# Kernel tuning notes

Hardware: AMD Instinct MI355X
Metric: run time of the kernel (lower is better)

Reference implementation:

```python
import jax, jax.numpy as jnp
import numpy as np

N_DIM, D_SKETCH, M_COLS = 8192, 1024, 4096


def setup_inputs() -> dict:
    key = jax.random.key(0)
    kM, kD, kP = jax.random.split(key, 3)
    M = jax.random.normal(kM, (N_DIM, M_COLS), dtype=jnp.float32)
    # Rademacher signs, exactly as 2*(rand > 0.5).float() - 1
    D = 2.0 * (jax.random.uniform(kD, (N_DIM,)) > 0.5).astype(jnp.float32) - 1.0
    # np.random.choice(N, d) samples with replacement -> plain randint
    P = jax.random.randint(kP, (D_SKETCH,), 0, N_DIM)
    return {"M": M, "D": D, "P": P}


def _idct_rows(X, rows):
    # torch_dct.idct with norm=None along the last axis, evaluated only at the
    # output positions `rows` (identical values to full idct followed by gather):
    #   x[n] = (1/N) * ( X[...,0]/2 + sum_{k=1}^{N-1} X[...,k] * cos(pi*(2n+1)*k/(2N)) )
    N = X.shape[-1]
    k = jnp.arange(N, dtype=jnp.float32)
    w = jnp.where(k == 0, 0.5, 1.0) / N                      # DCT-III weights / N
    n = rows.astype(jnp.float32)
    ang = (jnp.pi / (2.0 * N)) * (2.0 * n[:, None] + 1.0) * k[None, :]
    C = jnp.cos(ang) * w[None, :]                            # [d, N]
    return jnp.einsum('dk,mk->md', C, X)                     # [m, d]


def reference(M, D, P):
    # SRFT sketch, 2-D branch, transpose=False:
    #   result = idct((D[:, None] * M).T).T[P, :]   ->  shape [d, m]
    X = D[:, None] * M                                       # sign flip, [N, m]
    out = _idct_rows(X.T, P)                                 # [m, d]
    return out.T                                             # [d, m]
```

## Files before the change

### kernel.cpp

```cpp
#include <hip/hip_runtime.h>

#define K_DIM 8192
#define M_OUT 1024
#define N_OUT 4096
#define BUFSZ 49152

typedef __attribute__((ext_vector_type(4))) float f32x4;
typedef __attribute__((ext_vector_type(8))) __bf16 bf16x8;
typedef __attribute__((ext_vector_type(2))) __bf16 bf16x2;
typedef __attribute__((ext_vector_type(8))) unsigned short u16x8;

__device__ __forceinline__ unsigned short f2bf(float x) {
  unsigned u = __builtin_bit_cast(unsigned, x);
  u += 0x7fffu + ((u >> 16) & 1u);
  return (unsigned short)(u >> 16);
}

__device__ __forceinline__ unsigned pack2(float a, float b) {
  bf16x2 v;
  v[0] = (__bf16)a;
  v[1] = (__bf16)b;
  return __builtin_bit_cast(unsigned, v);
}

__global__ __launch_bounds__(256) void build_c_kernel(
    const int* __restrict__ Pp, const float* __restrict__ Dp,
    unsigned short* __restrict__ Cm) {
  const int p = blockIdx.x;
  const int n2 = 2 * Pp[p] + 1;
  const int t = threadIdx.x;
#pragma unroll
  for (int ch = 0; ch < 4; ++ch) {
    const int kb = (ch << 11) + (t << 3);
    u16x8 o;
#pragma unroll
    for (int i = 0; i < 8; ++i) {
      const int k = kb + i;
      const unsigned tt = ((unsigned)(n2 * k)) & 32767u;
      const float cv = cosf((float)tt * 1.9174759848570515e-4f);
      const float wk = (k == 0) ? (0.5f / 8192.0f) : (1.0f / 8192.0f);
      o[i] = f2bf(cv * wk * Dp[k]);
    }
    *(u16x8*)(Cm + ((size_t)p << 13) + kb) = o;
  }
}

__global__ __launch_bounds__(512, 2) void gemm_kernel(
    const unsigned short* __restrict__ Cm, const float* __restrict__ Mp,
    float* __restrict__ outp, int kchunk, int nwg) {
  __shared__ __align__(16) char lds[2 * BUFSZ];

  const int id = blockIdx.x;
  const int chunk = nwg >> 3;
  const int sid = (id & 7) * chunk + (id >> 3);
  const int bz = sid & 1, bm = (sid >> 1) & 3, bn = sid >> 3;

  const int t = threadIdx.x;
  const int w = t >> 6, l = t & 63;
  const int wr = w >> 1, wc = w & 1;
  const int lg = l >> 4, lr = l & 15;
  const int k_begin = bz * kchunk;
  const int NT = kchunk >> 6;

  const int arow = t >> 3;
  const int acol = ((t & 7) << 4) ^ ((arow & 7) << 4);
  const char* Agl = (const char*)Cm + ((size_t)(bm * 256 + arow) << 14) +
                    ((size_t)k_begin << 1) + acol;
  auto stageA = [&](int nbuf, int tile) {
    char* d = (char*)lds + nbuf * BUFSZ + t * 16;
    const char* s = Agl + ((size_t)tile << 7);
#pragma unroll
    for (int i = 0; i < 4; ++i)
      __builtin_amdgcn_global_load_lds(
          (const __attribute__((address_space(1))) void*)(s + ((size_t)i << 20)),
          (__attribute__((address_space(3))) void*)(d + i * 8192), 16, 0, 0);
  };

  const int bk0 = w * 8 + (l >> 5) * 4;
  const int bn0 = (l & 31) * 4;
  const float* Bg = Mp + (size_t)k_begin * N_OUT + bn * 128 + bn0;
  auto loadB = [&](f32x4 (&r)[4], int tile) {
#pragma unroll
    for (int i = 0; i < 4; ++i)
      r[i] = *(const f32x4*)(Bg + (size_t)(tile * 64 + bk0 + i) * N_OUT);
  };
  auto writeB = [&](const f32x4 (&r)[4], int nbuf) {
#pragma unroll
    for (int nn = 0; nn < 4; ++nn) {
      const int n = bn0 + nn;
      const int sN = (n & 7) ^ ((n >> 2) & 7);
      uint2 pk;
      pk.x = pack2(r[0][nn], r[1][nn]);
      pk.y = pack2(r[2][nn], r[3][nn]);
      *(uint2*)(lds + nbuf * BUFSZ + 32768 + n * 128 + ((w ^ sN) << 4) +
                ((l >> 5) << 3)) = pk;
    }
  };

  const int sw = (lr & 7) << 4;
  const int xk0 = (lg << 4) ^ sw;
  const int xk1 = (64 + (lg << 4)) ^ sw;
  unsigned boff[2][4];
#pragma unroll
  for (int kk = 0; kk < 2; ++kk)
#pragma unroll
    for (int nf = 0; nf < 4; ++nf) {
      const int row = wc * 64 + nf * 16 + lr;
      const int sN = (row & 7) ^ ((row >> 2) & 7);
      boff[kk][nf] = 32768 + row * 128 + ((((kk << 2) | lg) ^ sN) << 4);
    }

  f32x4 acc[4][4] = {};
  bf16x8 Af[4];
  bf16x8 Bf[4];

  auto readA = [&](int nbuf, int xk) {
    const char* aBuf = (const char*)lds + nbuf * BUFSZ + wr * 8192 + lr * 128;
#pragma unroll
    for (int m = 0; m < 4; ++m)
      Af[m] = *(const bf16x8*)(aBuf + m * 2048 + xk);
  };
  auto readB = [&](int nbuf, int kk) {
#pragma unroll
    for (int nf = 0; nf < 4; ++nf)
      Bf[nf] = *(const bf16x8*)(lds + nbuf * BUFSZ + boff[kk][nf]);
  };
  auto mm = [&]() {
    __builtin_amdgcn_s_setprio(1);
#pragma unroll
    for (int m = 0; m < 4; ++m)
#pragma unroll
      for (int nf = 0; nf < 4; ++nf)
        acc[m][nf] = __builtin_amdgcn_mfma_f32_16x16x32_bf16(
            Af[m], Bf[nf], acc[m][nf], 0, 0, 0);
    __builtin_amdgcn_s_setprio(0);
  };

  f32x4 sbA[4], sbB[4];

  {
    stageA(0, 0);
    loadB(sbB, 1);
    f32x4 p0[4];
    loadB(p0, 0);
    writeB(p0, 0);
    asm volatile("s_waitcnt vmcnt(0) lgkmcnt(0)" ::: "memory");
    __builtin_amdgcn_sched_barrier(0);
    __builtin_amdgcn_s_barrier();
  }

  auto tile_body = [&](int tt, f32x4 (&sbLoad)[4], f32x4 (&sbWrite)[4]) {
    const int cur = tt & 1, nxt = cur ^ 1;
    readA(cur, xk0);
    readB(cur, 0);
    if (tt + 1 < NT) stageA(nxt, tt + 1);
    if (tt + 2 < NT) loadB(sbLoad, tt + 2);
    __builtin_amdgcn_s_barrier();
    asm volatile("s_waitcnt lgkmcnt(0)" ::: "memory");
    __builtin_amdgcn_sched_barrier(0);
    mm();
    __builtin_amdgcn_s_barrier();
    readA(cur, xk1);
    readB(cur, 1);
    if (tt + 1 < NT) writeB(sbWrite, nxt);
    asm volatile("s_waitcnt lgkmcnt(0)" ::: "memory");
    __builtin_amdgcn_sched_barrier(0);
    mm();
    if (tt + 2 < NT) { asm volatile("s_waitcnt vmcnt(4)" ::: "memory"); }
    else             { asm volatile("s_waitcnt vmcnt(0)" ::: "memory"); }
    __builtin_amdgcn_sched_barrier(0);
    __builtin_amdgcn_s_barrier();
  };

  for (int tt = 0; tt < NT; tt += 2) {
    tile_body(tt, sbA, sbB);
    tile_body(tt + 1, sbB, sbA);
  }

  float* po = outp + (size_t)bz * (M_OUT * N_OUT);
  const int orow = bm * 256 + wr * 64;
  const int ocol = bn * 128 + wc * 64 + lr;
#pragma unroll
  for (int m = 0; m < 4; ++m) {
    const int r0 = orow + m * 16 + (lg << 2);
#pragma unroll
    for (int nf = 0; nf < 4; ++nf) {
      const int c = ocol + nf * 16;
#pragma unroll
      for (int q = 0; q < 4; ++q)
        po[(size_t)(r0 + q) * N_OUT + c] = acc[m][nf][q];
    }
  }
}

__global__ __launch_bounds__(256) void reduce_kernel(
    const float* __restrict__ part, float* __restrict__ out, int ksplit) {
  const size_t total = (size_t)M_OUT * N_OUT;
  const size_t i = ((size_t)blockIdx.x * 256 + threadIdx.x) * 4;
  if (i >= total) return;
  f32x4 s = *(const f32x4*)(part + i);
  for (int s2 = 1; s2 < ksplit; ++s2) s += *(const f32x4*)(part + (size_t)s2 * total + i);
  *(f32x4*)(out + i) = s;
}

__global__ __launch_bounds__(256) void naive_kernel(
    const float* __restrict__ Mp, const float* __restrict__ Dp,
    const int* __restrict__ Pp, float* __restrict__ out) {
  const int p = blockIdx.y;
  const int j = blockIdx.x * 256 + threadIdx.x;
  const int n2 = 2 * Pp[p] + 1;
  float acc = 0.0f;
  for (int k = 0; k < K_DIM; ++k) {
    const unsigned tt = ((unsigned)(n2 * k)) & 32767u;
    const float cv = cosf((float)tt * 1.9174759848570515e-4f);
    const float wk = (k == 0) ? 0.5f : 1.0f;
    acc += cv * wk * Dp[k] * Mp[(size_t)k * N_OUT + j];
  }
  out[(size_t)p * N_OUT + j] = acc * (1.0f / 8192.0f);
}

extern "C" void kernel_launch(void* const* d_in, const int* in_sizes, int n_in,
                              void* d_out, int out_size, void* d_ws, size_t ws_size,
                              hipStream_t stream) {
  const float* Mp = (const float*)d_in[0];
  const float* Dp = (const float*)d_in[1];
  const int* Pp = (const int*)d_in[2];
  float* out = (float*)d_out;

  const size_t CM_BYTES = (size_t)M_OUT * K_DIM * 2;
  const size_t PART_BYTES = (size_t)M_OUT * N_OUT * 4;

  int ksplit;
  if (ws_size >= CM_BYTES + 2 * PART_BYTES) ksplit = 2;
  else if (ws_size >= CM_BYTES) ksplit = 1;
  else ksplit = 0;

  if (ksplit == 0) {
    naive_kernel<<<dim3(N_OUT / 256, M_OUT), 256, 0, stream>>>(Mp, Dp, Pp, out);
    return;
  }

  unsigned short* Cm = (unsigned short*)d_ws;
  float* part = (float*)((char*)d_ws + CM_BYTES);

  build_c_kernel<<<dim3(M_OUT), 256, 0, stream>>>(Pp, Dp, Cm);

  float* gout = (ksplit > 1) ? part : out;
  const int kchunk = K_DIM / ksplit;
  const int nwg = (M_OUT / 256) * (N_OUT / 128) * ksplit;
  gemm_kernel<<<dim3(nwg), 512, 0, stream>>>(Cm, Mp, gout, kchunk, nwg);

  if (ksplit > 1)
    reduce_kernel<<<dim3((M_OUT * N_OUT / 4 + 255) / 256), 256, 0, stream>>>(part, out, ksplit);
}
```

Baseline: 123.4 us.

## Shrink GEMM tile to 128x128 and simplify pipeline for higher occupancy

Halves the workgroup M-tile from 256 to 128 rows, giving a 2x4 warp layout with 64x32 outputs per warp. LDS per buffer drops to 32 KB and launch bounds allow 4 workgroups per CU. The grid doubles to 512 workgroups, and the split-K index is now derived from a runtime ksplit. The two-deep register prefetch of B with partial vmcnt waits is replaced by a one-tile-ahead prefetch with one barrier per tile. This trades lower per-tile data reuse, since B is loaded twice as often, for better CU fill and latency hiding through occupancy.

```diff
diff --git a/kernel.cpp b/kernel.cpp
--- a/kernel.cpp
+++ b/kernel.cpp
@@ -3,7 +3,7 @@
 #define K_DIM 8192
 #define M_OUT 1024
 #define N_OUT 4096
-#define BUFSZ 49152
+#define BUFSZ 32768
 
 typedef __attribute__((ext_vector_type(4))) float f32x4;
 typedef __attribute__((ext_vector_type(8))) __bf16 bf16x8;
@@ -45,32 +45,34 @@
   }
 }
 
-__global__ __launch_bounds__(512, 2) void gemm_kernel(
+__global__ __launch_bounds__(512, 4) void gemm_kernel(
     const unsigned short* __restrict__ Cm, const float* __restrict__ Mp,
-    float* __restrict__ outp, int kchunk, int nwg) {
+    float* __restrict__ outp, int kchunk, int nwg, int ksplit) {
   __shared__ __align__(16) char lds[2 * BUFSZ];
 
   const int id = blockIdx.x;
   const int chunk = nwg >> 3;
   const int sid = (id & 7) * chunk + (id >> 3);
-  const int bz = sid & 1, bm = (sid >> 1) & 3, bn = sid >> 3;
+  const int bz = sid % ksplit;
+  const int rest = sid / ksplit;
+  const int bm = rest & 7, bn = rest >> 3;
 
   const int t = threadIdx.x;
   const int w = t >> 6, l = t & 63;
-  const int wr = w >> 1, wc = w & 1;
+  const int wr = w >> 2, wc = w & 3;
   const int lg = l >> 4, lr = l & 15;
   const int k_begin = bz * kchunk;
   const int NT = kchunk >> 6;
 
   const int arow = t >> 3;
   const int acol = ((t & 7) << 4) ^ ((arow & 7) << 4);
-  const char* Agl = (const char*)Cm + ((size_t)(bm * 256 + arow) << 14) +
+  const char* Agl = (const char*)Cm + ((size_t)(bm * 128 + arow) << 14) +
                     ((size_t)k_begin << 1) + acol;
   auto stageA = [&](int nbuf, int tile) {
     char* d = (char*)lds + nbuf * BUFSZ + t * 16;
     const char* s = Agl + ((size_t)tile << 7);
 #pragma unroll
-    for (int i = 0; i < 4; ++i)
+    for (int i = 0; i < 2; ++i)
       __builtin_amdgcn_global_load_lds(
           (const __attribute__((address_space(1))) void*)(s + ((size_t)i << 20)),
           (__attribute__((address_space(3))) void*)(d + i * 8192), 16, 0, 0);
@@ -92,7 +94,7 @@
       uint2 pk;
       pk.x = pack2(r[0][nn], r[1][nn]);
       pk.y = pack2(r[2][nn], r[3][nn]);
-      *(uint2*)(lds + nbuf * BUFSZ + 32768 + n * 128 + ((w ^ sN) << 4) +
+      *(uint2*)(lds + nbuf * BUFSZ + 16384 + n * 128 + ((w ^ sN) << 4) +
                 ((l >> 5) << 3)) = pk;
     }
   };
@@ -100,19 +102,19 @@
   const int sw = (lr & 7) << 4;
   const int xk0 = (lg << 4) ^ sw;
   const int xk1 = (64 + (lg << 4)) ^ sw;
-  unsigned boff[2][4];
+  unsigned boff[2][2];
 #pragma unroll
   for (int kk = 0; kk < 2; ++kk)
 #pragma unroll
-    for (int nf = 0; nf < 4; ++nf) {
-      const int row = wc * 64 + nf * 16 + lr;
+    for (int nf = 0; nf < 2; ++nf) {
+      const int row = wc * 32 + nf * 16 + lr;
       const int sN = (row & 7) ^ ((row >> 2) & 7);
-      boff[kk][nf] = 32768 + row * 128 + ((((kk << 2) | lg) ^ sN) << 4);
-    }
-
-  f32x4 acc[4][4] = {};
+      boff[kk][nf] = 16384 + row * 128 + ((((kk << 2) | lg) ^ sN) << 4);
+    }
+
+  f32x4 acc[4][2] = {};
   bf16x8 Af[4];
-  bf16x8 Bf[4];
+  bf16x8 Bf[2];
 
   auto readA = [&](int nbuf, int xk) {
     const char* aBuf = (const char*)lds + nbuf * BUFSZ + wr * 8192 + lr * 128;
@@ -122,7 +124,7 @@
   };
   auto readB = [&](int nbuf, int kk) {
 #pragma unroll
-    for (int nf = 0; nf < 4; ++nf)
+    for (int nf = 0; nf < 2; ++nf)
       Bf[nf] = *(const bf16x8*)(lds + nbuf * BUFSZ + boff[kk][nf]);
   };
   auto mm = [&]() {
@@ -130,18 +132,15 @@
 #pragma unroll
     for (int m = 0; m < 4; ++m)
 #pragma unroll
-      for (int nf = 0; nf < 4; ++nf)
+      for (int nf = 0; nf < 2; ++nf)
         acc[m][nf] = __builtin_amdgcn_mfma_f32_16x16x32_bf16(
             Af[m], Bf[nf], acc[m][nf], 0, 0, 0);
     __builtin_amdgcn_s_setprio(0);
   };
 
-  f32x4 sbA[4], sbB[4];
-
   {
+    f32x4 p0[4];
     stageA(0, 0);
-    loadB(sbB, 1);
-    f32x4 p0[4];
     loadB(p0, 0);
     writeB(p0, 0);
     asm volatile("s_waitcnt vmcnt(0) lgkmcnt(0)" ::: "memory");
@@ -149,42 +148,34 @@
     __builtin_amdgcn_s_barrier();
   }
 
-  auto tile_body = [&](int tt, f32x4 (&sbLoad)[4], f32x4 (&sbWrite)[4]) {
+  for (int tt = 0; tt < NT; ++tt) {
     const int cur = tt & 1, nxt = cur ^ 1;
+    const bool more = (tt + 1) < NT;
+    f32x4 sb[4];
+    if (more) {
+      loadB(sb, tt + 1);
+      stageA(nxt, tt + 1);
+    }
+    readB(cur, 0);
     readA(cur, xk0);
-    readB(cur, 0);
-    if (tt + 1 < NT) stageA(nxt, tt + 1);
-    if (tt + 2 < NT) loadB(sbLoad, tt + 2);
-    __builtin_amdgcn_s_barrier();
-    asm volatile("s_waitcnt lgkmcnt(0)" ::: "memory");
-    __builtin_amdgcn_sched_barrier(0);
     mm();
-    __builtin_amdgcn_s_barrier();
+    if (more) writeB(sb, nxt);
+    readB(cur, 1);
     readA(cur, xk1);
-    readB(cur, 1);
-    if (tt + 1 < NT) writeB(sbWrite, nxt);
-    asm volatile("s_waitcnt lgkmcnt(0)" ::: "memory");
-    __builtin_amdgcn_sched_barrier(0);
     mm();
-    if (tt + 2 < NT) { asm volatile("s_waitcnt vmcnt(4)" ::: "memory"); }
-    else             { asm volatile("s_waitcnt vmcnt(0)" ::: "memory"); }
+    asm volatile("s_waitcnt vmcnt(0) lgkmcnt(0)" ::: "memory");
     __builtin_amdgcn_sched_barrier(0);
     __builtin_amdgcn_s_barrier();
-  };
-
-  for (int tt = 0; tt < NT; tt += 2) {
-    tile_body(tt, sbA, sbB);
-    tile_body(tt + 1, sbB, sbA);
   }
 
   float* po = outp + (size_t)bz * (M_OUT * N_OUT);
-  const int orow = bm * 256 + wr * 64;
-  const int ocol = bn * 128 + wc * 64 + lr;
+  const int orow = bm * 128 + wr * 64;
+  const int ocol = bn * 128 + wc * 32 + lr;
 #pragma unroll
   for (int m = 0; m < 4; ++m) {
     const int r0 = orow + m * 16 + (lg << 2);
 #pragma unroll
-    for (int nf = 0; nf < 4; ++nf) {
+    for (int nf = 0; nf < 2; ++nf) {
       const int c = ocol + nf * 16;
 #pragma unroll
       for (int q = 0; q < 4; ++q)
@@ -247,8 +238,8 @@
 
   float* gout = (ksplit > 1) ? part : out;
   const int kchunk = K_DIM / ksplit;
-  const int nwg = (M_OUT / 256) * (N_OUT / 128) * ksplit;
-  gemm_kernel<<<dim3(nwg), 512, 0, stream>>>(Cm, Mp, gout, kchunk, nwg);
+  const int nwg = (M_OUT / 128) * (N_OUT / 128) * ksplit;
+  gemm_kernel<<<dim3(nwg), 512, 0, stream>>>(Cm, Mp, gout, kchunk, nwg, ksplit);
 
   if (ksplit > 1)
     reduce_kernel<<<dim3((M_OUT * N_OUT / 4 + 255) / 256), 256, 0, stream>>>(part, out, ksplit);
```

Result: faster. 118.9 us (-3.7%).
